# Kernel optimization log

Hardware: AMD Instinct MI355X
Metric: run time of the kernel (lower is better)

The kernel has to match this reference:

```python
import jax, jax.numpy as jnp
import numpy as np

B, S, H, NH = 2, 2048, 2048, 16
HD = H // NH  # 128
ROPE_BASE = 10000.0


def _rope(q, k, position_ids):
    # q, k: [B, NH, S, HD]; position_ids: [B, S]
    half = HD // 2
    inv_freq = 1.0 / (ROPE_BASE ** (jnp.arange(0, half, dtype=jnp.float32) / half))
    freqs = position_ids.astype(jnp.float32)[:, :, None] * inv_freq[None, None, :]  # [B,S,half]
    emb = jnp.concatenate([freqs, freqs], axis=-1)                                   # [B,S,HD]
    cos = jnp.cos(emb)[:, None, :, :]  # [B,1,S,HD]
    sin = jnp.sin(emb)[:, None, :, :]

    def rot_half(x):
        x1, x2 = jnp.split(x, 2, axis=-1)
        return jnp.concatenate([-x2, x1], axis=-1)

    q = q * cos + rot_half(q) * sin
    k = k * cos + rot_half(k) * sin
    return q, k


def setup_inputs() -> dict:
    key = jax.random.key(0)
    k1, k2, k3 = jax.random.split(key, 3)
    hidden_states = jax.random.normal(k1, (B, S, H), dtype=jnp.float32)
    position_ids = jnp.broadcast_to(jnp.arange(S, dtype=jnp.int32), (B, S))
    # additive causal mask (large finite negative to avoid inf arithmetic)
    causal = jnp.triu(jnp.full((S, S), -1e9, dtype=jnp.float32), k=1)
    attention_mask = jnp.broadcast_to(causal[None, None], (B, 1, S, S))
    qkv_w = jax.random.normal(k2, (3 * H, H), dtype=jnp.float32) * (H ** -0.5)
    qkv_b = jnp.zeros((3 * H,), dtype=jnp.float32)
    o_w = jax.random.normal(k3, (H, H), dtype=jnp.float32) * (H ** -0.5)
    return {"hidden_states": hidden_states, "position_ids": position_ids,
            "attention_mask": attention_mask, "qkv_w": qkv_w, "qkv_b": qkv_b, "o_w": o_w}


def reference(hidden_states, position_ids, attention_mask, qkv_w, qkv_b, o_w):
    qkv = hidden_states @ qkv_w.T + qkv_b                      # [B,S,3H]
    q, k, v = jnp.split(qkv, 3, axis=-1)

    def to_heads(x):
        return x.reshape(B, S, NH, HD).transpose(0, 2, 1, 3)   # [B,NH,S,HD]

    q, k, v = to_heads(q), to_heads(k), to_heads(v)
    q, k = _rope(q, k, position_ids)

    scale = 1.0 / np.sqrt(HD)
    scores = jnp.einsum('bhqd,bhkd->bhqk', q, k * scale)
    scores = scores + attention_mask
    probs = jax.nn.softmax(scores.astype(jnp.float32), axis=-1).astype(q.dtype)
    attn = jnp.einsum('bhqk,bhkd->bhqd', probs, v)
    attn = attn.transpose(0, 2, 1, 3).reshape(B, S, H)
    return attn @ o_w.T
```

## Files before the change

kernel.cpp:

```cpp
#include <hip/hip_runtime.h>
#include <hip/hip_bf16.h>

#define BB 2
#define SS 2048
#define HH 2048
#define NHH 16
#define HDD 128

using f32x4  = __attribute__((ext_vector_type(4))) float;
using bf16x8 = __attribute__((ext_vector_type(8))) short;

__device__ __forceinline__ unsigned short f2bf(float x) {
  unsigned int u = __float_as_uint(x);
  unsigned int r = (u + 0x7FFFu + ((u >> 16) & 1u)) >> 16;
  return (unsigned short)r;
}
__device__ __forceinline__ float bf2f(unsigned short u) {
  return __uint_as_float(((unsigned int)u) << 16);
}

__device__ __forceinline__ void gll16(const void* g, void* l) {
  __builtin_amdgcn_global_load_lds(
      (__attribute__((address_space(1))) void*)(g),
      (__attribute__((address_space(3))) void*)(l), 16, 0, 0);
}

#define MFMA16(a, b, c) __builtin_amdgcn_mfma_f32_16x16x32_bf16(a, b, c, 0, 0, 0)

template<int N> __device__ __forceinline__ void wlgkm() {
  static_assert(N == 0 || N == 2 || N == 4 || N == 6 || N == 8 || N == 10 || N == 12,
                "unsupported lgkmcnt");
  if constexpr (N == 0)       asm volatile("s_waitcnt lgkmcnt(0)"  ::: "memory");
  else if constexpr (N == 2)  asm volatile("s_waitcnt lgkmcnt(2)"  ::: "memory");
  else if constexpr (N == 4)  asm volatile("s_waitcnt lgkmcnt(4)"  ::: "memory");
  else if constexpr (N == 6)  asm volatile("s_waitcnt lgkmcnt(6)"  ::: "memory");
  else if constexpr (N == 8)  asm volatile("s_waitcnt lgkmcnt(8)"  ::: "memory");
  else if constexpr (N == 10) asm volatile("s_waitcnt lgkmcnt(10)" ::: "memory");
  else if constexpr (N == 12) asm volatile("s_waitcnt lgkmcnt(12)" ::: "memory");
}
template<int N> __device__ __forceinline__ void wvm() {
  static_assert(N == 0 || N == 5 || N == 6 || N == 7 || N == 8, "unsupported vmcnt");
  if constexpr (N == 0)      asm volatile("s_waitcnt vmcnt(0)" ::: "memory");
  else if constexpr (N == 5) asm volatile("s_waitcnt vmcnt(5)" ::: "memory");
  else if constexpr (N == 6) asm volatile("s_waitcnt vmcnt(6)" ::: "memory");
  else if constexpr (N == 7) asm volatile("s_waitcnt vmcnt(7)" ::: "memory");
  else if constexpr (N == 8) asm volatile("s_waitcnt vmcnt(8)" ::: "memory");
}


__global__ void convert_bf16(const float* __restrict__ in, unsigned short* __restrict__ out, int n4) {
  int i = blockIdx.x * blockDim.x + threadIdx.x;
  if (i >= n4) return;
  float4 v = reinterpret_cast<const float4*>(in)[i];
  ushort4 o;
  o.x = f2bf(v.x); o.y = f2bf(v.y); o.z = f2bf(v.z); o.w = f2bf(v.w);
  reinterpret_cast<ushort4*>(out)[i] = o;
}

__global__ void build_tab(float* __restrict__ tab) {
  int i = blockIdx.x * blockDim.x + threadIdx.x;
  if (i >= SS * 64) return;
  int s = i >> 6, j = i & 63;
  float invf = expf(-logf(10000.f) * ((float)j / 64.f));
  float a = (float)s * invf;
  tab[i * 2]     = cosf(a);
  tab[i * 2 + 1] = sinf(a);
}


__global__ __launch_bounds__(256)
void gemm_qkv97(const unsigned short* __restrict__ A,
                const unsigned short* __restrict__ Bw,
                const float* __restrict__ bias,
                unsigned short* __restrict__ outQ,
                unsigned short* __restrict__ outK,
                unsigned short* __restrict__ outV,
                int Kdim) {
  __shared__ unsigned short lA[128 * 64];
  __shared__ unsigned short lB[128 * 64];
  const int tid = threadIdx.x;
  const int tn = blockIdx.x, tm = blockIdx.y;
  const int wid = tid >> 6, lane = tid & 63;
  const int wm = wid >> 1, wn = wid & 1;
  const int lr = lane & 15, lg = lane >> 4;

  const unsigned short* Ab = A + (size_t)tm * 128 * Kdim;
  const unsigned short* Bb = Bw + (size_t)tn * 128 * Kdim;

  f32x4 acc[4][4] = {};

  const unsigned short* sa[4];
  const unsigned short* sb[4];
  unsigned short* da[4];
  unsigned short* db[4];
#pragma unroll
  for (int p = 0; p < 4; ++p) {
    int cl = p * 256 + tid;
    int ri = cl >> 3, c = cl & 7;
    int cg = c ^ (ri & 7);
    sa[p] = Ab + (size_t)ri * Kdim + (cg << 3);
    sb[p] = Bb + (size_t)ri * Kdim + (cg << 3);
    da[p] = lA + ri * 64 + (c << 3);
    db[p] = lB + ri * 64 + (c << 3);
  }

  const int nt = Kdim >> 6;

  for (int k = 0; k < nt; ++k) {
#pragma unroll
    for (int p = 0; p < 4; ++p) {
      gll16(sa[p], da[p]); sa[p] += 64;
      gll16(sb[p], db[p]); sb[p] += 64;
    }
    __syncthreads();

    bf16x8 af[4][2], bf[4][2];
#pragma unroll
    for (int t = 0; t < 4; ++t) {
      int ra = wm * 64 + t * 16 + lr;
      int rb = wn * 64 + t * 16 + lr;
      af[t][0] = *reinterpret_cast<const bf16x8*>(lA + ra * 64 + ((lg ^ (ra & 7)) << 3));
      af[t][1] = *reinterpret_cast<const bf16x8*>(lA + ra * 64 + (((4 + lg) ^ (ra & 7)) << 3));
      bf[t][0] = *reinterpret_cast<const bf16x8*>(lB + rb * 64 + ((lg ^ (rb & 7)) << 3));
      bf[t][1] = *reinterpret_cast<const bf16x8*>(lB + rb * 64 + (((4 + lg) ^ (rb & 7)) << 3));
    }
#pragma unroll
    for (int i = 0; i < 4; ++i)
#pragma unroll
      for (int j = 0; j < 4; ++j) {
        acc[i][j] = MFMA16(af[i][0], bf[j][0], acc[i][j]);
        acc[i][j] = MFMA16(af[i][1], bf[j][1], acc[i][j]);
      }
    __syncthreads();
  }

#pragma unroll
  for (int i = 0; i < 4; ++i) {
#pragma unroll
    for (int j = 0; j < 4; ++j) {
      int n = tn * 128 + wn * 64 + j * 16 + lr;
#pragma unroll
      for (int r = 0; r < 4; ++r) {
        int m = tm * 128 + wm * 64 + i * 16 + lg * 4 + r;
        float v = acc[i][j][r] + bias[n];
        int sel = n >> 11;
        int h = (n >> 7) & 15;
        int d = n & 127;
        int b = m >> 11;
        int s = m & 2047;
        if (sel == 0)
          outQ[(((size_t)(b * 16 + h)) * 2048 + s) * 128 + d] = f2bf(v);
        else if (sel == 1)
          outK[(((size_t)(b * 16 + h)) * 2048 + s) * 128 + d] = f2bf(v);
        else
          outV[(((size_t)(b * 16 + h)) * 128 + d) * 2048 + s] = f2bf(v);
      }
    }
  }
}


template<int MODE, int MI, int NB>
__global__ __launch_bounds__(512, 1)
void gemm_pipe(const unsigned short* __restrict__ A,
               const unsigned short* __restrict__ Bw,
               const float* __restrict__ bias,
               float* __restrict__ outF,
               unsigned short* __restrict__ outQ,
               unsigned short* __restrict__ outK,
               unsigned short* __restrict__ outV,
               int Kdim) {
  constexpr int BM = 32 * MI;
  constexpr int BN = 64 * NB;
  constexpr int TOPS = 2 * (BM / 128) + NB;
  __shared__ unsigned short lA[2][BM * 64];
  __shared__ unsigned short lB[2][BN * 64];
  const int tid = threadIdx.x;
  const int tn = blockIdx.x, tm = blockIdx.y;
  const int wid = tid >> 6, lane = tid & 63;
  const int wm = wid >> 2, wn = wid & 3;
  const int lr = lane & 15, lg = lane >> 4;

  const unsigned short* Ab = A + (size_t)tm * BM * Kdim;
  const unsigned short* Bb = Bw + (size_t)tn * BN * Kdim;

  f32x4 acc[MI][NB] = {};
  bf16x8 af[MI][2], bfr[NB][2];

  const int nt = Kdim >> 6;

  auto stageA = [&](int t, int h) {
    unsigned short* L = lA[t & 1];
    const int k0 = t << 6;
#pragma unroll
    for (int p = 0; p < BM / 128; ++p) {
      int cl = p * 512 + tid;
      int ri = cl >> 3, c = cl & 7;
      int row = (ri / (8 * MI)) * (16 * MI) + h * (8 * MI) + (ri % (8 * MI));
      int cg = c ^ (row & 7);
      gll16(Ab + (size_t)row * Kdim + k0 + (cg << 3), L + row * 64 + (c << 3));
    }
  };
  auto stageB = [&](int t, int h) {
    unsigned short* L = lB[t & 1];
    const int k0 = t << 6;
    int cl = tid;
    int ri = cl >> 3, c = cl & 7;
    int row = (ri >> 4) * (16 * NB) + h * 16 + (ri & 15);
    int cg = c ^ (row & 7);
    gll16(Bb + (size_t)row * Kdim + k0 + (cg << 3), L + row * 64 + (c << 3));
  };
  auto readAhalf = [&](int g, int h) {
    const unsigned short* la = lA[g & 1];
#pragma unroll
    for (int mi = h * (MI / 2); mi < (h + 1) * (MI / 2); ++mi) {
      int ra = wm * (BM / 2) + mi * 16 + lr;
      af[mi][0] = *reinterpret_cast<const bf16x8*>(la + ra * 64 + ((lg ^ (ra & 7)) << 3));
      af[mi][1] = *reinterpret_cast<const bf16x8*>(la + ra * 64 + (((4 + lg) ^ (ra & 7)) << 3));
    }
  };
  auto readB = [&](int g, int ni) {
    const unsigned short* lb = lB[g & 1];
    int rb = wn * (16 * NB) + ni * 16 + lr;
    bfr[ni][0] = *reinterpret_cast<const bf16x8*>(lb + rb * 64 + ((lg ^ (rb & 7)) << 3));
    bfr[ni][1] = *reinterpret_cast<const bf16x8*>(lb + rb * 64 + (((4 + lg) ^ (rb & 7)) << 3));
  };
  auto quad = [&](int ah, int ni) {
    __builtin_amdgcn_s_setprio(1);
#pragma unroll
    for (int mi = ah * (MI / 2); mi < (ah + 1) * (MI / 2); ++mi) {
      acc[mi][ni] = MFMA16(af[mi][0], bfr[ni][0], acc[mi][ni]);
      acc[mi][ni] = MFMA16(af[mi][1], bfr[ni][1], acc[mi][ni]);
    }
    __builtin_amdgcn_s_setprio(0);
  };

  stageA(0, 0); stageA(0, 1);
#pragma unroll
  for (int h = 0; h < NB; ++h) stageB(0, h);
  stageA(1, 0); stageA(1, 1);
#pragma unroll
  for (int h = 0; h < NB; ++h) stageB(1, h);
  wvm<TOPS>();
  __builtin_amdgcn_s_barrier();
  __builtin_amdgcn_sched_barrier(0);
  readAhalf(0, 0);
#pragma unroll
  for (int ni = 0; ni < NB - 1; ++ni) readB(0, ni);

  for (int g = 0; g < nt; ++g) {
    readB(g, NB - 1);
    wlgkm<2 * (NB - 1)>();
    __builtin_amdgcn_sched_barrier(0);
    quad(0, 0);

    readAhalf(g, 1);
    wlgkm<2 * (NB - 2) + MI>();
    __builtin_amdgcn_sched_barrier(0);
    quad(0, 1);

    if constexpr (NB == 4) {
      wlgkm<2 + MI>();
      __builtin_amdgcn_sched_barrier(0);
      quad(0, 2);
    }

    wlgkm<MI>();
    __builtin_amdgcn_sched_barrier(0);
    quad(0, NB - 1);

    asm volatile("s_waitcnt vmcnt(0) lgkmcnt(0)" ::: "memory");
    __builtin_amdgcn_s_barrier();
    __builtin_amdgcn_sched_barrier(0);
    if (g + 1 < nt) readAhalf(g + 1, 0);
    if (g + 2 < nt) { stageA(g + 2, 0); stageA(g + 2, 1); }
    quad(1, 0);

    if (g + 1 < nt) readB(g + 1, 0);
    if (g + 2 < nt) {
#pragma unroll
      for (int h = 0; h < NB; ++h) stageB(g + 2, h);
    }
    quad(1, 1);

    if (g + 1 < nt) readB(g + 1, 1);
    quad(1, 2);
    if constexpr (NB == 4) {
      if (g + 1 < nt) readB(g + 1, 2);
      quad(1, 3);
    }
  }

#pragma unroll
  for (int mi = 0; mi < MI; ++mi) {
#pragma unroll
    for (int ni = 0; ni < NB; ++ni) {
      int n = tn * BN + wn * (16 * NB) + ni * 16 + lr;
#pragma unroll
      for (int r = 0; r < 4; ++r) {
        int m = tm * BM + wm * (BM / 2) + mi * 16 + lg * 4 + r;
        float v = acc[mi][ni][r];
        if (MODE == 1) {
          v += bias[n];
          int sel = n >> 11;
          int h = (n >> 7) & 15;
          int d = n & 127;
          int b = m >> 11;
          int s = m & 2047;
          if (sel == 0)
            outQ[(((size_t)(b * 16 + h)) * 2048 + s) * 128 + d] = f2bf(v);
          else if (sel == 1)
            outK[(((size_t)(b * 16 + h)) * 2048 + s) * 128 + d] = f2bf(v);
          else
            outV[(((size_t)(b * 16 + h)) * 128 + d) * 2048 + s] = f2bf(v);
        } else {
          outF[(size_t)m * 2048 + n] = v;
        }
      }
    }
  }
}


__global__ void rope_inplace(unsigned short* __restrict__ Qr, unsigned short* __restrict__ Kr,
                             const int* __restrict__ pos, const float* __restrict__ tab) {
  int i = blockIdx.x * blockDim.x + threadIdx.x;
  if (i >= (1 << 20)) return;
  int jb = i & 7;
  int s  = (i >> 3) & 2047;
  int bh = (i >> 14) & 31;
  int a  = i >> 19;
  unsigned short* base = (a ? Kr : Qr) + (((size_t)bh * 2048 + s) * 128);
  int b = bh >> 4;
  int p = pos[b * 2048 + s];
  bf16x8 x1 = *reinterpret_cast<bf16x8*>(base + jb * 8);
  bf16x8 x2 = *reinterpret_cast<bf16x8*>(base + 64 + jb * 8);
  bf16x8 y1, y2;
#pragma unroll
  for (int t = 0; t < 8; ++t) {
    int j = jb * 8 + t;
    float c  = tab[((size_t)p * 64 + j) * 2];
    float sn = tab[((size_t)p * 64 + j) * 2 + 1];
    float a1 = bf2f((unsigned short)x1[t]);
    float a2 = bf2f((unsigned short)x2[t]);
    y1[t] = (short)f2bf(a1 * c - a2 * sn);
    y2[t] = (short)f2bf(a2 * c + a1 * sn);
  }
  *reinterpret_cast<bf16x8*>(base + jb * 8) = y1;
  *reinterpret_cast<bf16x8*>(base + 64 + jb * 8) = y2;
}


__global__ __launch_bounds__(256)
void attn_fwd(const unsigned short* __restrict__ Qr,
              const unsigned short* __restrict__ Kr,
              const unsigned short* __restrict__ Vt,
              unsigned short* __restrict__ attnb) {
  __shared__ unsigned short Ks[2][64 * 128];
  __shared__ unsigned short Vs[2][128 * 64];
  __shared__ unsigned short Ps[64 * 64];
  const int bx = blockIdx.x, bh = blockIdx.y;
  const int tid = threadIdx.x;
  const int wid = tid >> 6, lane = tid & 63;
  const int lr = lane & 15, lg = lane >> 4;
  const unsigned short* Qb = Qr + (size_t)bh * SS * HDD;
  const unsigned short* Kb = Kr + (size_t)bh * SS * HDD;
  const unsigned short* Vb = Vt + (size_t)bh * HDD * SS;
  const int b = bh >> 4, h = bh & 15;

  auto stage = [&](int kt, int buf) {
#pragma unroll
    for (int ch = 0; ch < 4; ++ch) {
      int c = tid + ch * 256;
      {
        int row = c >> 4, cb = c & 15;
        gll16(Kb + ((size_t)(kt * 64 + row)) * 128 + ((cb ^ (row & 7)) << 3), Ks[buf] + c * 8);
      }
      {
        int row = c >> 3, cb = c & 7;
        gll16(Vb + (size_t)row * SS + kt * 64 + ((cb ^ (row & 7)) << 3), Vs[buf] + c * 8);
      }
    }
  };

#pragma unroll 1
  for (int qi = 0; qi < 2; ++qi) {
    const int qt = qi ? bx : (31 - bx);

    bf16x8 qf[4];
#pragma unroll
    for (int kk = 0; kk < 4; ++kk)
      qf[kk] = *reinterpret_cast<const bf16x8*>(
          Qb + ((size_t)(qt * 64 + wid * 16 + lr)) * 128 + kk * 32 + lg * 8);

    f32x4 oacc[8] = {};
    float mrow[4], lsum[4];
#pragma unroll
    for (int r = 0; r < 4; ++r) { mrow[r] = -1e30f; lsum[r] = 0.f; }

    int cur = 0;
    stage(0, 0);

#pragma unroll 1
    for (int kt = 0; kt <= qt; ++kt) {
      if (kt < qt) {
        stage(kt + 1, cur ^ 1);
        asm volatile("s_waitcnt vmcnt(8)" ::: "memory");
      } else {
        asm volatile("s_waitcnt vmcnt(0)" ::: "memory");
      }
      __builtin_amdgcn_s_barrier();
      __builtin_amdgcn_sched_barrier(0);

      float sv[4][4];
#pragma unroll
      for (int nt = 0; nt < 4; ++nt) {
        f32x4 sa = {};
#pragma unroll
        for (int kk = 0; kk < 4; ++kk) {
          int row = nt * 16 + lr;
          bf16x8 kf = *reinterpret_cast<const bf16x8*>(
              Ks[cur] + row * 128 + (((kk * 4 + lg) ^ (row & 7)) << 3));
          sa = __builtin_amdgcn_mfma_f32_16x16x32_bf16(qf[kk], kf, sa, 0, 0, 0);
        }
#pragma unroll
        for (int r = 0; r < 4; ++r) {
          float s = sa[r] * 0.088388347648318447f;
          if (kt == qt && (nt * 16 + lr) > (wid * 16 + lg * 4 + r)) s -= 1e9f;
          sv[nt][r] = s;
        }
      }

      float tmax[4];
#pragma unroll
      for (int r = 0; r < 4; ++r)
        tmax[r] = fmaxf(fmaxf(sv[0][r], sv[1][r]), fmaxf(sv[2][r], sv[3][r]));
#pragma unroll
      for (int r = 0; r < 4; ++r) {
        tmax[r] = fmaxf(tmax[r], __shfl_xor(tmax[r], 1));
        tmax[r] = fmaxf(tmax[r], __shfl_xor(tmax[r], 2));
        tmax[r] = fmaxf(tmax[r], __shfl_xor(tmax[r], 4));
        tmax[r] = fmaxf(tmax[r], __shfl_xor(tmax[r], 8));
      }
      float fr[4], tsum[4];
#pragma unroll
      for (int r = 0; r < 4; ++r) {
        float mn = fmaxf(mrow[r], tmax[r]);
        fr[r] = __expf(mrow[r] - mn);
        mrow[r] = mn;
        tsum[r] = 0.f;
      }
#pragma unroll
      for (int nt = 0; nt < 4; ++nt) {
        int colc = nt * 2 + (lr >> 3);
#pragma unroll
        for (int r = 0; r < 4; ++r) {
          float p = __expf(sv[nt][r] - mrow[r]);
          tsum[r] += p;
          int row = wid * 16 + lg * 4 + r;
          Ps[row * 64 + ((colc ^ (row & 7)) << 3) + (lr & 7)] = f2bf(p);
        }
      }
#pragma unroll
      for (int r = 0; r < 4; ++r) {
        tsum[r] += __shfl_xor(tsum[r], 1);
        tsum[r] += __shfl_xor(tsum[r], 2);
        tsum[r] += __shfl_xor(tsum[r], 4);
        tsum[r] += __shfl_xor(tsum[r], 8);
        lsum[r] = lsum[r] * fr[r] + tsum[r];
      }
#pragma unroll
      for (int ct = 0; ct < 8; ++ct)
#pragma unroll
        for (int r = 0; r < 4; ++r)
          oacc[ct][r] *= fr[r];

      bf16x8 pf[2];
#pragma unroll
      for (int ks = 0; ks < 2; ++ks) {
        int row = wid * 16 + lr;
        pf[ks] = *reinterpret_cast<const bf16x8*>(
            Ps + row * 64 + (((ks * 4 + lg) ^ (row & 7)) << 3));
      }
#pragma unroll
      for (int ct = 0; ct < 8; ++ct) {
#pragma unroll
        for (int ks = 0; ks < 2; ++ks) {
          int row = ct * 16 + lr;
          bf16x8 vf = *reinterpret_cast<const bf16x8*>(
              Vs[cur] + row * 64 + (((ks * 4 + lg) ^ (row & 7)) << 3));
          oacc[ct] = __builtin_amdgcn_mfma_f32_16x16x32_bf16(pf[ks], vf, oacc[ct], 0, 0, 0);
        }
      }
      __builtin_amdgcn_s_barrier();
      cur ^= 1;
    }

#pragma unroll
    for (int r = 0; r < 4; ++r) {
      float rl = 1.f / lsum[r];
      int qg = qt * 64 + wid * 16 + lg * 4 + r;
#pragma unroll
      for (int ct = 0; ct < 8; ++ct) {
        int d = ct * 16 + lr;
        attnb[((size_t)b * SS + qg) * HH + h * 128 + d] = f2bf(oacc[ct][r] * rl);
      }
    }
  }
}


extern "C" void kernel_launch(void* const* d_in, const int* in_sizes, int n_in,
                              void* d_out, int out_size, void* d_ws, size_t ws_size,
                              hipStream_t stream) {
  const float* hs     = (const float*)d_in[0];
  const int*   pos    = (const int*)d_in[1];
  const float* qkv_w  = (const float*)d_in[3];
  const float* qkv_b  = (const float*)d_in[4];
  const float* o_w    = (const float*)d_in[5];
  float* out = (float*)d_out;
  char* ws = (char*)d_ws;

  unsigned short* hsb   = (unsigned short*)(ws);
  unsigned short* wqkvb = (unsigned short*)(ws + 16777216);
  unsigned short* owb   = (unsigned short*)(ws + 41943040);
  unsigned short* Qr    = (unsigned short*)(ws + 50331648);
  unsigned short* Kr    = (unsigned short*)(ws + 67108864);
  unsigned short* Vt    = (unsigned short*)(ws + 83886080);
  unsigned short* attnb = (unsigned short*)(ws + 100663296);
  float*          tab   = (float*)(ws + 117440512);

  convert_bf16<<<2097152 / 256, 256, 0, stream>>>(hs, hsb, 2097152);
  convert_bf16<<<3145728 / 256, 256, 0, stream>>>(qkv_w, wqkvb, 3145728);
  convert_bf16<<<1048576 / 256, 256, 0, stream>>>(o_w, owb, 1048576);
  build_tab<<<512, 256, 0, stream>>>(tab);

  gemm_qkv97<<<dim3(48, 32), 256, 0, stream>>>(hsb, wqkvb, qkv_b, Qr, Kr, Vt, 2048);
  rope_inplace<<<4096, 256, 0, stream>>>(Qr, Kr, pos, tab);
  attn_fwd<<<dim3(16, 32), 256, 0, stream>>>(Qr, Kr, Vt, attnb);
  gemm_pipe<0, 4, 4><<<dim3(8, 32), 512, 0, stream>>>(attnb, owb, nullptr, out, nullptr, nullptr, nullptr, 2048);
}
```

Before: 329.6 us.

## Swap GEMM kernels between QKV and output, add lazy softmax rescale

The QKV projection now uses the pipelined 512-thread GEMM with 256x256 tiles, and the output projection uses the simpler 128x128 kernel, generalised with a MODE template. The attention kernel precomputes K/V load addresses and advances pointers instead of recomputing them each tile. It also skips the online-softmax rescale of the accumulator unless some row's max rises by more than 8, which removes exp and multiply work per tile. The lazy rescale risks fp32 overflow only in extreme cases, and the larger tiles change occupancy and wave counts.

After: 309.9 us. 1.06x faster.

```diff
diff --git a/kernel.cpp b/kernel.cpp
--- a/kernel.cpp
+++ b/kernel.cpp
@@ -68,99 +68,7 @@
 }
 
 
-__global__ __launch_bounds__(256)
-void gemm_qkv97(const unsigned short* __restrict__ A,
-                const unsigned short* __restrict__ Bw,
-                const float* __restrict__ bias,
-                unsigned short* __restrict__ outQ,
-                unsigned short* __restrict__ outK,
-                unsigned short* __restrict__ outV,
-                int Kdim) {
-  __shared__ unsigned short lA[128 * 64];
-  __shared__ unsigned short lB[128 * 64];
-  const int tid = threadIdx.x;
-  const int tn = blockIdx.x, tm = blockIdx.y;
-  const int wid = tid >> 6, lane = tid & 63;
-  const int wm = wid >> 1, wn = wid & 1;
-  const int lr = lane & 15, lg = lane >> 4;
-
-  const unsigned short* Ab = A + (size_t)tm * 128 * Kdim;
-  const unsigned short* Bb = Bw + (size_t)tn * 128 * Kdim;
-
-  f32x4 acc[4][4] = {};
-
-  const unsigned short* sa[4];
-  const unsigned short* sb[4];
-  unsigned short* da[4];
-  unsigned short* db[4];
-#pragma unroll
-  for (int p = 0; p < 4; ++p) {
-    int cl = p * 256 + tid;
-    int ri = cl >> 3, c = cl & 7;
-    int cg = c ^ (ri & 7);
-    sa[p] = Ab + (size_t)ri * Kdim + (cg << 3);
-    sb[p] = Bb + (size_t)ri * Kdim + (cg << 3);
-    da[p] = lA + ri * 64 + (c << 3);
-    db[p] = lB + ri * 64 + (c << 3);
-  }
-
-  const int nt = Kdim >> 6;
-
-  for (int k = 0; k < nt; ++k) {
-#pragma unroll
-    for (int p = 0; p < 4; ++p) {
-      gll16(sa[p], da[p]); sa[p] += 64;
-      gll16(sb[p], db[p]); sb[p] += 64;
-    }
-    __syncthreads();
-
-    bf16x8 af[4][2], bf[4][2];
-#pragma unroll
-    for (int t = 0; t < 4; ++t) {
-      int ra = wm * 64 + t * 16 + lr;
-      int rb = wn * 64 + t * 16 + lr;
-      af[t][0] = *reinterpret_cast<const bf16x8*>(lA + ra * 64 + ((lg ^ (ra & 7)) << 3));
-      af[t][1] = *reinterpret_cast<const bf16x8*>(lA + ra * 64 + (((4 + lg) ^ (ra & 7)) << 3));
-      bf[t][0] = *reinterpret_cast<const bf16x8*>(lB + rb * 64 + ((lg ^ (rb & 7)) << 3));
-      bf[t][1] = *reinterpret_cast<const bf16x8*>(lB + rb * 64 + (((4 + lg) ^ (rb & 7)) << 3));
-    }
-#pragma unroll
-    for (int i = 0; i < 4; ++i)
-#pragma unroll
-      for (int j = 0; j < 4; ++j) {
-        acc[i][j] = MFMA16(af[i][0], bf[j][0], acc[i][j]);
-        acc[i][j] = MFMA16(af[i][1], bf[j][1], acc[i][j]);
-      }
-    __syncthreads();
-  }
-
-#pragma unroll
-  for (int i = 0; i < 4; ++i) {
-#pragma unroll
-    for (int j = 0; j < 4; ++j) {
-      int n = tn * 128 + wn * 64 + j * 16 + lr;
-#pragma unroll
-      for (int r = 0; r < 4; ++r) {
-        int m = tm * 128 + wm * 64 + i * 16 + lg * 4 + r;
-        float v = acc[i][j][r] + bias[n];
-        int sel = n >> 11;
-        int h = (n >> 7) & 15;
-        int d = n & 127;
-        int b = m >> 11;
-        int s = m & 2047;
-        if (sel == 0)
-          outQ[(((size_t)(b * 16 + h)) * 2048 + s) * 128 + d] = f2bf(v);
-        else if (sel == 1)
-          outK[(((size_t)(b * 16 + h)) * 2048 + s) * 128 + d] = f2bf(v);
-        else
-          outV[(((size_t)(b * 16 + h)) * 128 + d) * 2048 + s] = f2bf(v);
-      }
-    }
-  }
-}
-
-
-template<int MODE, int MI, int NB>
+template<int MODE, int MI>
 __global__ __launch_bounds__(512, 1)
 void gemm_pipe(const unsigned short* __restrict__ A,
                const unsigned short* __restrict__ Bw,
@@ -171,10 +79,8 @@
                unsigned short* __restrict__ outV,
                int Kdim) {
   constexpr int BM = 32 * MI;
-  constexpr int BN = 64 * NB;
-  constexpr int TOPS = 2 * (BM / 128) + NB;
   __shared__ unsigned short lA[2][BM * 64];
-  __shared__ unsigned short lB[2][BN * 64];
+  __shared__ unsigned short lB[2][256 * 64];
   const int tid = threadIdx.x;
   const int tn = blockIdx.x, tm = blockIdx.y;
   const int wid = tid >> 6, lane = tid & 63;
@@ -182,10 +88,10 @@
   const int lr = lane & 15, lg = lane >> 4;
 
   const unsigned short* Ab = A + (size_t)tm * BM * Kdim;
-  const unsigned short* Bb = Bw + (size_t)tn * BN * Kdim;
-
-  f32x4 acc[MI][NB] = {};
-  bf16x8 af[MI][2], bfr[NB][2];
+  const unsigned short* Bb = Bw + (size_t)tn * 256 * Kdim;
+
+  f32x4 acc[MI][4] = {};
+  bf16x8 af[MI][2], bfr[4][2];
 
   const int nt = Kdim >> 6;
 
@@ -204,11 +110,14 @@
   auto stageB = [&](int t, int h) {
     unsigned short* L = lB[t & 1];
     const int k0 = t << 6;
-    int cl = tid;
-    int ri = cl >> 3, c = cl & 7;
-    int row = (ri >> 4) * (16 * NB) + h * 16 + (ri & 15);
-    int cg = c ^ (row & 7);
-    gll16(Bb + (size_t)row * Kdim + k0 + (cg << 3), L + row * 64 + (c << 3));
+#pragma unroll
+    for (int p = 0; p < 2; ++p) {
+      int cl = p * 512 + tid;
+      int ri = cl >> 3, c = cl & 7;
+      int row = (ri >> 5 << 6) + (h << 5) + (ri & 31);
+      int cg = c ^ (row & 7);
+      gll16(Bb + (size_t)row * Kdim + k0 + (cg << 3), L + row * 64 + (c << 3));
+    }
   };
   auto readAhalf = [&](int g, int h) {
     const unsigned short* la = lA[g & 1];
@@ -219,55 +128,46 @@
       af[mi][1] = *reinterpret_cast<const bf16x8*>(la + ra * 64 + (((4 + lg) ^ (ra & 7)) << 3));
     }
   };
-  auto readB = [&](int g, int ni) {
+  auto readBhalf = [&](int g, int h) {
     const unsigned short* lb = lB[g & 1];
-    int rb = wn * (16 * NB) + ni * 16 + lr;
-    bfr[ni][0] = *reinterpret_cast<const bf16x8*>(lb + rb * 64 + ((lg ^ (rb & 7)) << 3));
-    bfr[ni][1] = *reinterpret_cast<const bf16x8*>(lb + rb * 64 + (((4 + lg) ^ (rb & 7)) << 3));
+#pragma unroll
+    for (int ni = h * 2; ni < h * 2 + 2; ++ni) {
+      int rb = wn * 64 + ni * 16 + lr;
+      bfr[ni][0] = *reinterpret_cast<const bf16x8*>(lb + rb * 64 + ((lg ^ (rb & 7)) << 3));
+      bfr[ni][1] = *reinterpret_cast<const bf16x8*>(lb + rb * 64 + (((4 + lg) ^ (rb & 7)) << 3));
+    }
   };
-  auto quad = [&](int ah, int ni) {
+  auto quad = [&](int ah, int bh) {
     __builtin_amdgcn_s_setprio(1);
 #pragma unroll
-    for (int mi = ah * (MI / 2); mi < (ah + 1) * (MI / 2); ++mi) {
-      acc[mi][ni] = MFMA16(af[mi][0], bfr[ni][0], acc[mi][ni]);
-      acc[mi][ni] = MFMA16(af[mi][1], bfr[ni][1], acc[mi][ni]);
-    }
+    for (int mi = ah * (MI / 2); mi < (ah + 1) * (MI / 2); ++mi)
+#pragma unroll
+      for (int ni = bh * 2; ni < bh * 2 + 2; ++ni) {
+        acc[mi][ni] = MFMA16(af[mi][0], bfr[ni][0], acc[mi][ni]);
+        acc[mi][ni] = MFMA16(af[mi][1], bfr[ni][1], acc[mi][ni]);
+      }
     __builtin_amdgcn_s_setprio(0);
   };
 
-  stageA(0, 0); stageA(0, 1);
-#pragma unroll
-  for (int h = 0; h < NB; ++h) stageB(0, h);
-  stageA(1, 0); stageA(1, 1);
-#pragma unroll
-  for (int h = 0; h < NB; ++h) stageB(1, h);
-  wvm<TOPS>();
+  stageA(0, 0); stageA(0, 1); stageB(0, 0); stageB(0, 1);
+  stageA(1, 0); stageA(1, 1); stageB(1, 0); stageB(1, 1);
+  if constexpr (MI == 8) wvm<8>();
+  else                   wvm<6>();
   __builtin_amdgcn_s_barrier();
   __builtin_amdgcn_sched_barrier(0);
   readAhalf(0, 0);
-#pragma unroll
-  for (int ni = 0; ni < NB - 1; ++ni) readB(0, ni);
+  readBhalf(0, 0);
 
   for (int g = 0; g < nt; ++g) {
-    readB(g, NB - 1);
-    wlgkm<2 * (NB - 1)>();
+    readBhalf(g, 1);
+    wlgkm<4>();
     __builtin_amdgcn_sched_barrier(0);
     quad(0, 0);
 
     readAhalf(g, 1);
-    wlgkm<2 * (NB - 2) + MI>();
+    if constexpr (MI == 8) wlgkm<8>(); else wlgkm<4>();
     __builtin_amdgcn_sched_barrier(0);
     quad(0, 1);
-
-    if constexpr (NB == 4) {
-      wlgkm<2 + MI>();
-      __builtin_amdgcn_sched_barrier(0);
-      quad(0, 2);
-    }
-
-    wlgkm<MI>();
-    __builtin_amdgcn_sched_barrier(0);
-    quad(0, NB - 1);
 
     asm volatile("s_waitcnt vmcnt(0) lgkmcnt(0)" ::: "memory");
     __builtin_amdgcn_s_barrier();
@@ -276,26 +176,16 @@
     if (g + 2 < nt) { stageA(g + 2, 0); stageA(g + 2, 1); }
     quad(1, 0);
 
-    if (g + 1 < nt) readB(g + 1, 0);
-    if (g + 2 < nt) {
-#pragma unroll
-      for (int h = 0; h < NB; ++h) stageB(g + 2, h);
-    }
+    if (g + 1 < nt) readBhalf(g + 1, 0);
+    if (g + 2 < nt) { stageB(g + 2, 0); stageB(g + 2, 1); }
     quad(1, 1);
-
-    if (g + 1 < nt) readB(g + 1, 1);
-    quad(1, 2);
-    if constexpr (NB == 4) {
-      if (g + 1 < nt) readB(g + 1, 2);
-      quad(1, 3);
-    }
   }
 
 #pragma unroll
   for (int mi = 0; mi < MI; ++mi) {
 #pragma unroll
-    for (int ni = 0; ni < NB; ++ni) {
-      int n = tn * BN + wn * (16 * NB) + ni * 16 + lr;
+    for (int ni = 0; ni < 4; ++ni) {
+      int n = tn * 256 + wn * 64 + ni * 16 + lr;
 #pragma unroll
       for (int r = 0; r < 4; ++r) {
         int m = tm * BM + wm * (BM / 2) + mi * 16 + lg * 4 + r;
@@ -322,6 +212,105 @@
 }
 
 
+template<int MODE>
+__global__ __launch_bounds__(256)
+void gemm97(const unsigned short* __restrict__ A,
+            const unsigned short* __restrict__ Bw,
+            const float* __restrict__ bias,
+            float* __restrict__ outF,
+            unsigned short* __restrict__ outQ,
+            unsigned short* __restrict__ outK,
+            unsigned short* __restrict__ outV,
+            int Kdim) {
+  __shared__ unsigned short lA[128 * 64];
+  __shared__ unsigned short lB[128 * 64];
+  const int tid = threadIdx.x;
+  const int tn = blockIdx.x, tm = blockIdx.y;
+  const int wid = tid >> 6, lane = tid & 63;
+  const int wm = wid >> 1, wn = wid & 1;
+  const int lr = lane & 15, lg = lane >> 4;
+
+  const unsigned short* Ab = A + (size_t)tm * 128 * Kdim;
+  const unsigned short* Bb = Bw + (size_t)tn * 128 * Kdim;
+
+  f32x4 acc[4][4] = {};
+
+  const unsigned short* sa[4];
+  const unsigned short* sb[4];
+  unsigned short* da[4];
+  unsigned short* db[4];
+#pragma unroll
+  for (int p = 0; p < 4; ++p) {
+    int cl = p * 256 + tid;
+    int ri = cl >> 3, c = cl & 7;
+    int cg = c ^ (ri & 7);
+    sa[p] = Ab + (size_t)ri * Kdim + (cg << 3);
+    sb[p] = Bb + (size_t)ri * Kdim + (cg << 3);
+    da[p] = lA + ri * 64 + (c << 3);
+    db[p] = lB + ri * 64 + (c << 3);
+  }
+
+  const int nt = Kdim >> 6;
+
+  for (int k = 0; k < nt; ++k) {
+#pragma unroll
+    for (int p = 0; p < 4; ++p) {
+      gll16(sa[p], da[p]); sa[p] += 64;
+      gll16(sb[p], db[p]); sb[p] += 64;
+    }
+    __syncthreads();
+
+    bf16x8 af[4][2], bf[4][2];
+#pragma unroll
+    for (int t = 0; t < 4; ++t) {
+      int ra = wm * 64 + t * 16 + lr;
+      int rb = wn * 64 + t * 16 + lr;
+      af[t][0] = *reinterpret_cast<const bf16x8*>(lA + ra * 64 + ((lg ^ (ra & 7)) << 3));
+      af[t][1] = *reinterpret_cast<const bf16x8*>(lA + ra * 64 + (((4 + lg) ^ (ra & 7)) << 3));
+      bf[t][0] = *reinterpret_cast<const bf16x8*>(lB + rb * 64 + ((lg ^ (rb & 7)) << 3));
+      bf[t][1] = *reinterpret_cast<const bf16x8*>(lB + rb * 64 + (((4 + lg) ^ (rb & 7)) << 3));
+    }
+#pragma unroll
+    for (int i = 0; i < 4; ++i)
+#pragma unroll
+      for (int j = 0; j < 4; ++j) {
+        acc[i][j] = MFMA16(af[i][0], bf[j][0], acc[i][j]);
+        acc[i][j] = MFMA16(af[i][1], bf[j][1], acc[i][j]);
+      }
+    __syncthreads();
+  }
+
+#pragma unroll
+  for (int i = 0; i < 4; ++i) {
+#pragma unroll
+    for (int j = 0; j < 4; ++j) {
+      int n = tn * 128 + wn * 64 + j * 16 + lr;
+#pragma unroll
+      for (int r = 0; r < 4; ++r) {
+        int m = tm * 128 + wm * 64 + i * 16 + lg * 4 + r;
+        float v = acc[i][j][r];
+        if (MODE == 1) {
+          v += bias[n];
+          int sel = n >> 11;
+          int h = (n >> 7) & 15;
+          int d = n & 127;
+          int b = m >> 11;
+          int s = m & 2047;
+          if (sel == 0)
+            outQ[(((size_t)(b * 16 + h)) * 2048 + s) * 128 + d] = f2bf(v);
+          else if (sel == 1)
+            outK[(((size_t)(b * 16 + h)) * 2048 + s) * 128 + d] = f2bf(v);
+          else
+            outV[(((size_t)(b * 16 + h)) * 128 + d) * 2048 + s] = f2bf(v);
+        } else {
+          outF[(size_t)m * 2048 + n] = v;
+        }
+      }
+    }
+  }
+}
+
+
 __global__ void rope_inplace(unsigned short* __restrict__ Qr, unsigned short* __restrict__ Kr,
                              const int* __restrict__ pos, const float* __restrict__ tab) {
   int i = blockIdx.x * blockDim.x + threadIdx.x;
@@ -368,18 +357,26 @@
   const unsigned short* Vb = Vt + (size_t)bh * HDD * SS;
   const int b = bh >> 4, h = bh & 15;
 
-  auto stage = [&](int kt, int buf) {
+  const unsigned short* ksrc0[4];
+  const unsigned short* vsrc0[4];
+  int dst8[4];
+#pragma unroll
+  for (int ch = 0; ch < 4; ++ch) {
+    int c = tid + ch * 256;
+    int kr = c >> 4, kc = c & 15;
+    ksrc0[ch] = Kb + (size_t)kr * 128 + ((kc ^ (kr & 7)) << 3);
+    int vr = c >> 3, vc = c & 7;
+    vsrc0[ch] = Vb + (size_t)vr * SS + ((vc ^ (vr & 7)) << 3);
+    dst8[ch] = c * 8;
+  }
+  const unsigned short* ksrc[4];
+  const unsigned short* vsrc[4];
+
+  auto stage = [&](int buf) {
 #pragma unroll
     for (int ch = 0; ch < 4; ++ch) {
-      int c = tid + ch * 256;
-      {
-        int row = c >> 4, cb = c & 15;
-        gll16(Kb + ((size_t)(kt * 64 + row)) * 128 + ((cb ^ (row & 7)) << 3), Ks[buf] + c * 8);
-      }
-      {
-        int row = c >> 3, cb = c & 7;
-        gll16(Vb + (size_t)row * SS + kt * 64 + ((cb ^ (row & 7)) << 3), Vs[buf] + c * 8);
-      }
+      gll16(ksrc[ch], Ks[buf] + dst8[ch]); ksrc[ch] += 64 * 128;
+      gll16(vsrc[ch], Vs[buf] + dst8[ch]); vsrc[ch] += 64;
     }
   };
 
@@ -387,6 +384,9 @@
   for (int qi = 0; qi < 2; ++qi) {
     const int qt = qi ? bx : (31 - bx);
 
+#pragma unroll
+    for (int ch = 0; ch < 4; ++ch) { ksrc[ch] = ksrc0[ch]; vsrc[ch] = vsrc0[ch]; }
+
     bf16x8 qf[4];
 #pragma unroll
     for (int kk = 0; kk < 4; ++kk)
@@ -399,12 +399,12 @@
     for (int r = 0; r < 4; ++r) { mrow[r] = -1e30f; lsum[r] = 0.f; }
 
     int cur = 0;
-    stage(0, 0);
+    stage(0);
 
 #pragma unroll 1
     for (int kt = 0; kt <= qt; ++kt) {
       if (kt < qt) {
-        stage(kt + 1, cur ^ 1);
+        stage(cur ^ 1);
         asm volatile("s_waitcnt vmcnt(8)" ::: "memory");
       } else {
         asm volatile("s_waitcnt vmcnt(0)" ::: "memory");
@@ -442,14 +442,22 @@
         tmax[r] = fmaxf(tmax[r], __shfl_xor(tmax[r], 4));
         tmax[r] = fmaxf(tmax[r], __shfl_xor(tmax[r], 8));
       }
-      float fr[4], tsum[4];
-#pragma unroll
-      for (int r = 0; r < 4; ++r) {
-        float mn = fmaxf(mrow[r], tmax[r]);
-        fr[r] = __expf(mrow[r] - mn);
-        mrow[r] = mn;
-        tsum[r] = 0.f;
-      }
+
+      float need = fmaxf(fmaxf(tmax[0] - mrow[0], tmax[1] - mrow[1]),
+                         fmaxf(tmax[2] - mrow[2], tmax[3] - mrow[3]));
+      if (__any(need > 8.f)) {
+#pragma unroll
+        for (int r = 0; r < 4; ++r) {
+          float mn = fmaxf(mrow[r], tmax[r]);
+          float fr = __expf(mrow[r] - mn);
+          mrow[r] = mn;
+          lsum[r] *= fr;
+#pragma unroll
+          for (int ct = 0; ct < 8; ++ct) oacc[ct][r] *= fr;
+        }
+      }
+
+      float tsum[4] = {0.f, 0.f, 0.f, 0.f};
 #pragma unroll
       for (int nt = 0; nt < 4; ++nt) {
         int colc = nt * 2 + (lr >> 3);
@@ -467,13 +475,8 @@
         tsum[r] += __shfl_xor(tsum[r], 2);
         tsum[r] += __shfl_xor(tsum[r], 4);
         tsum[r] += __shfl_xor(tsum[r], 8);
-        lsum[r] = lsum[r] * fr[r] + tsum[r];
-      }
-#pragma unroll
-      for (int ct = 0; ct < 8; ++ct)
-#pragma unroll
-        for (int r = 0; r < 4; ++r)
-          oacc[ct][r] *= fr[r];
+        lsum[r] += tsum[r];
+      }
 
       bf16x8 pf[2];
 #pragma unroll
@@ -535,8 +538,8 @@
   convert_bf16<<<1048576 / 256, 256, 0, stream>>>(o_w, owb, 1048576);
   build_tab<<<512, 256, 0, stream>>>(tab);
 
-  gemm_qkv97<<<dim3(48, 32), 256, 0, stream>>>(hsb, wqkvb, qkv_b, Qr, Kr, Vt, 2048);
+  gemm_pipe<1, 8><<<dim3(24, 16), 512, 0, stream>>>(hsb, wqkvb, qkv_b, nullptr, Qr, Kr, Vt, 2048);
   rope_inplace<<<4096, 256, 0, stream>>>(Qr, Kr, pos, tab);
   attn_fwd<<<dim3(16, 32), 256, 0, stream>>>(Qr, Kr, Vt, attnb);
-  gemm_pipe<0, 4, 4><<<dim3(8, 32), 512, 0, stream>>>(attnb, owb, nullptr, out, nullptr, nullptr, nullptr, 2048);
-}
+  gemm97<0><<<dim3(16, 32), 256, 0, stream>>>(attnb, owb, nullptr, out, nullptr, nullptr, nullptr, 2048);
+}
```
